# Performance work log

Hardware: AMD Instinct MI355X
Metric: run time of the kernel (lower is better)

## Reference

```python
import jax, jax.numpy as jnp
import numpy as np

TOP_K = 4
NORM_TOPK_PROB = True


def _moe_forward(hidden_states, Wr, Wg, Wu, Wd):
    # hidden_states: [B, S, H]; Wr: [E, H]; Wg/Wu: [E, F, H]; Wd: [E, H, F]
    B, S, H = hidden_states.shape
    E = Wr.shape[0]
    x = hidden_states.reshape(-1, H)                     # [T, H]
    T = x.shape[0]

    # Router: softmax in float32 (matches F.softmax(..., dtype=torch.float))
    router_logits = x @ Wr.T                              # [T, E]
    probs = jax.nn.softmax(router_logits.astype(jnp.float32), axis=-1)
    routing_weights, selected_experts = jax.lax.top_k(probs, TOP_K)  # [T, K]
    if NORM_TOPK_PROB:
        routing_weights = routing_weights / jnp.sum(routing_weights, axis=-1, keepdims=True)
    routing_weights = routing_weights.astype(x.dtype)

    # Dense combine matrix: combine[t, e] = routing weight if expert e selected for token t else 0.
    # Equivalent to the sort/gather dispatch + weighted scatter-add in the torch code.
    combine = jnp.zeros((T, E), dtype=x.dtype).at[
        jnp.arange(T)[:, None], selected_experts
    ].add(routing_weights)                               # [T, E]

    # SwiGLU expert MLP: down(silu(gate(x)) * up(x)), evaluated for all experts,
    # then masked/weighted by combine (zero weight == token not routed to expert).
    hg = jnp.einsum('td,efd->tef', x, Wg)                # [T, E, F]
    hu = jnp.einsum('td,efd->tef', x, Wu)                # [T, E, F]
    act = jax.nn.silu(hg) * hu                           # [T, E, F]
    out = jnp.einsum('tef,te,edf->td', act, combine, Wd) # [T, H]
    return out.reshape(B, S, H)


def setup_inputs() -> dict:
    key = jax.random.key(0)
    k0, k1, k2, k3, k4 = jax.random.split(key, 5)
    B, S, H, E, F = 2, 2048, 2048, 16, 768
    scale = 0.02
    return {
        'hidden_states': jax.random.normal(k0, (B, S, H), dtype=jnp.float32),
        'Wr': jax.random.normal(k1, (E, H), dtype=jnp.float32) * scale,
        'Wg': jax.random.normal(k2, (E, F, H), dtype=jnp.float32) * scale,
        'Wu': jax.random.normal(k3, (E, F, H), dtype=jnp.float32) * scale,
        'Wd': jax.random.normal(k4, (E, H, F), dtype=jnp.float32) * scale,
    }


def reference(hidden_states, Wr, Wg, Wu, Wd):
    return _moe_forward(hidden_states, Wr, Wg, Wu, Wd)
```

## Files before the change

### kernel.cpp

```cpp
#include <hip/hip_runtime.h>
#include <hip/hip_bf16.h>

#define H_DIM 2048
#define F_DIM 768
#define E_NUM 16
#define T_TOK 4096
#define TOPK  4
#define TK_ROWS (T_TOK * TOPK)

typedef __attribute__((ext_vector_type(8))) short bf16x8;
typedef __attribute__((ext_vector_type(4))) float f32x4;

static __device__ __forceinline__ float bf2f(unsigned short u) {
    return __uint_as_float(((unsigned)u) << 16);
}
static __device__ __forceinline__ unsigned short f2bu(float f) {
    __hip_bfloat16 h = __float2bfloat16(f);
    return *(unsigned short*)&h;
}

static __device__ __forceinline__ void stage8(unsigned short* dst, const void* src,
                                              size_t eoff, bool f32) {
    if (f32) {
        const float* s = (const float*)src + eoff;
        float4 a = *(const float4*)s;
        float4 b = *(const float4*)(s + 4);
        __align__(16) unsigned short u[8] = {
            f2bu(a.x), f2bu(a.y), f2bu(a.z), f2bu(a.w),
            f2bu(b.x), f2bu(b.y), f2bu(b.z), f2bu(b.w)};
        *(uint4*)dst = *(const uint4*)u;
    } else {
        *(uint4*)dst = *(const uint4*)((const unsigned short*)src + eoff);
    }
}

__global__ void probe_kernel(const unsigned short* __restrict__ wr, int* __restrict__ flag) {
    const int tid = threadIdx.x;
    int maxe = 0;
    for (int i = tid; i < 512; i += 64) {
        int e = (wr[i] >> 7) & 0xFF;
        maxe = max(maxe, e);
    }
    for (int off = 32; off > 0; off >>= 1)
        maxe = max(maxe, __shfl_down(maxe, off, 64));
    if (tid == 0) flag[0] = (maxe >= 135) ? 1 : 0;
}

__global__ __launch_bounds__(256)
void convert_kernel(unsigned short* __restrict__ dst, const void* __restrict__ src,
                    const int* __restrict__ dflag, size_t n) {
    const size_t i = ((size_t)blockIdx.x * 256 + threadIdx.x) * 8;
    if (i >= n) return;
    stage8(dst + i, src, i, dflag[0] != 0);
}

__global__ __launch_bounds__(256)
void router_kernel(const void* __restrict__ xv,
                   const void* __restrict__ wrv,
                   const int* __restrict__ dflag,
                   float* __restrict__ topk_w,
                   int* __restrict__ topk_e,
                   int* __restrict__ counts) {
    const bool f32 = dflag[0] != 0;
    const int t = blockIdx.x;
    __shared__ float xs[H_DIM];
    __shared__ float logits_s[E_NUM];
    const int tid = threadIdx.x;

    if (f32) {
        const float4* xr = (const float4*)((const float*)xv + (size_t)t * H_DIM);
        ((float4*)xs)[tid] = xr[tid];
        ((float4*)xs)[tid + 256] = xr[tid + 256];
    } else {
        const uint4* xr = (const uint4*)((const unsigned short*)xv + (size_t)t * H_DIM);
        uint4 b = xr[tid];
        const unsigned short* bp = (const unsigned short*)&b;
#pragma unroll
        for (int j = 0; j < 8; ++j) xs[tid * 8 + j] = bf2f(bp[j]);
    }
    __syncthreads();

    const int w = tid >> 6;
    const int lane = tid & 63;

    float acc[4] = {0.f, 0.f, 0.f, 0.f};
    for (int i = 0; i < 4; ++i) {
        const int h = i * 512 + lane * 8;
        float xf[8];
#pragma unroll
        for (int j = 0; j < 8; ++j) xf[j] = xs[h + j];
#pragma unroll
        for (int je = 0; je < 4; ++je) {
            const int e = w * 4 + je;
            float wf[8];
            if (f32) {
                const float* wp = (const float*)wrv + (size_t)e * H_DIM + h;
                float4 a = *(const float4*)wp;
                float4 b = *(const float4*)(wp + 4);
                wf[0]=a.x; wf[1]=a.y; wf[2]=a.z; wf[3]=a.w;
                wf[4]=b.x; wf[5]=b.y; wf[6]=b.z; wf[7]=b.w;
            } else {
                uint4 wb = *(const uint4*)((const unsigned short*)wrv + (size_t)e * H_DIM + h);
                const unsigned short* wp = (const unsigned short*)&wb;
#pragma unroll
                for (int j = 0; j < 8; ++j) wf[j] = bf2f(wp[j]);
            }
            float s = 0.f;
#pragma unroll
            for (int j = 0; j < 8; ++j) s += xf[j] * wf[j];
            acc[je] += s;
        }
    }
#pragma unroll
    for (int je = 0; je < 4; ++je) {
        float v = acc[je];
        for (int off = 32; off > 0; off >>= 1) v += __shfl_down(v, off, 64);
        if (lane == 0) logits_s[w * 4 + je] = v;
    }
    __syncthreads();

    if (tid == 0) {
        float l[E_NUM];
#pragma unroll
        for (int i = 0; i < E_NUM; ++i) l[i] = logits_s[i];
        unsigned mask = 0;
        int sel_e[TOPK];
        float sel_v[TOPK];
        for (int k = 0; k < TOPK; ++k) {
            int be = 0; float bv = -1e30f;
            for (int i = 0; i < E_NUM; ++i) {
                if (!(mask & (1u << i)) && l[i] > bv) { bv = l[i]; be = i; }
            }
            mask |= (1u << be);
            sel_e[k] = be; sel_v[k] = bv;
        }
        const float m = sel_v[0];
        float ex[TOPK]; float s = 0.f;
        for (int k = 0; k < TOPK; ++k) { ex[k] = __expf(sel_v[k] - m); s += ex[k]; }
        const float inv = 1.f / s;
        for (int k = 0; k < TOPK; ++k) {
            float wgt = ex[k] * inv;
            if (!f32) wgt = bf2f(f2bu(wgt));
            topk_w[t * TOPK + k] = wgt;
            topk_e[t * TOPK + k] = sel_e[k];
            atomicAdd(&counts[sel_e[k]], 1);
        }
    }
}

__global__ void scan_kernel(const int* __restrict__ counts, int* __restrict__ offsets) {
    if (threadIdx.x == 0) {
        int s = 0;
        for (int e = 0; e < E_NUM; ++e) { offsets[e] = s; s += counts[e]; }
        offsets[E_NUM] = s;
    }
}

__global__ __launch_bounds__(256)
void scatter_kernel(const int* __restrict__ topk_e, const int* __restrict__ offsets,
                    int* __restrict__ cursors, int* __restrict__ row_token) {
    const int i = blockIdx.x * 256 + threadIdx.x;
    if (i < TK_ROWS) {
        const int e = topk_e[i];
        const int pos = offsets[e] + atomicAdd(&cursors[e], 1);
        row_token[pos] = i;
    }
}

__global__ __launch_bounds__(256, 2)
void gateup_kernel(const void* __restrict__ xv,
                   const void* __restrict__ wgv,
                   const void* __restrict__ wuv,
                   const int* __restrict__ dflag,
                   const int* __restrict__ row_token,
                   const int* __restrict__ counts,
                   const int* __restrict__ offsets,
                   __hip_bfloat16* __restrict__ act_buf) {
    const bool f32 = dflag[0] != 0;
    const int e  = blockIdx.z;
    const int mt = blockIdx.y;
    const int ft = blockIdx.x;
    const int cnt = counts[e];
    if (mt * 128 >= cnt) return;
    const int base = offsets[e];

    __shared__ unsigned short As[128 * 72];
    __shared__ unsigned short Bgs[128 * 72];
    __shared__ unsigned short Bus[128 * 72];
    __shared__ int tok_s[128];

    const int tid = threadIdx.x;
    if (tid < 128) {
        int r = mt * 128 + tid;
        int gr = base + (r < cnt ? r : cnt - 1);
        tok_s[tid] = row_token[gr] >> 2;
    }
    __syncthreads();

    f32x4 accg[4][4], accu[4][4];
#pragma unroll
    for (int mi = 0; mi < 4; ++mi)
#pragma unroll
        for (int ni = 0; ni < 4; ++ni)
#pragma unroll
            for (int r = 0; r < 4; ++r) { accg[mi][ni][r] = 0.f; accu[mi][ni][r] = 0.f; }

    const int wid  = tid >> 6;
    const int lane = tid & 63;
    const int wm = (wid >> 1) * 64;
    const int wn = (wid & 1) * 64;
    const int lr = lane & 15;
    const int lq = lane >> 4;

    const int lrow = tid >> 3;
    const int lcol = (tid & 7) * 8;

    const size_t gOff = ((size_t)e * F_DIM + ft * 128) * H_DIM;

    for (int kk = 0; kk < H_DIM / 64; ++kk) {
        const int k0 = kk * 64;
#pragma unroll
        for (int rep = 0; rep < 4; ++rep) {
            const int row = lrow + rep * 32;
            stage8(&As[row * 72 + lcol],  xv,  (size_t)tok_s[row] * H_DIM + k0 + lcol, f32);
            stage8(&Bgs[row * 72 + lcol], wgv, gOff + (size_t)row * H_DIM + k0 + lcol, f32);
            stage8(&Bus[row * 72 + lcol], wuv, gOff + (size_t)row * H_DIM + k0 + lcol, f32);
        }
        __syncthreads();
#pragma unroll
        for (int ks = 0; ks < 2; ++ks) {
            const int kb = ks * 32 + lq * 8;
            bf16x8 a[4], bg[4], bu[4];
#pragma unroll
            for (int mi = 0; mi < 4; ++mi)
                a[mi] = *(const bf16x8*)&As[(wm + mi * 16 + lr) * 72 + kb];
#pragma unroll
            for (int ni = 0; ni < 4; ++ni) {
                bg[ni] = *(const bf16x8*)&Bgs[(wn + ni * 16 + lr) * 72 + kb];
                bu[ni] = *(const bf16x8*)&Bus[(wn + ni * 16 + lr) * 72 + kb];
            }
#pragma unroll
            for (int mi = 0; mi < 4; ++mi)
#pragma unroll
                for (int ni = 0; ni < 4; ++ni) {
                    accg[mi][ni] = __builtin_amdgcn_mfma_f32_16x16x32_bf16(a[mi], bg[ni], accg[mi][ni], 0, 0, 0);
                    accu[mi][ni] = __builtin_amdgcn_mfma_f32_16x16x32_bf16(a[mi], bu[ni], accu[mi][ni], 0, 0, 0);
                }
        }
        __syncthreads();
    }

#pragma unroll
    for (int mi = 0; mi < 4; ++mi) {
#pragma unroll
        for (int r = 0; r < 4; ++r) {
            const int row  = wm + mi * 16 + lq * 4 + r;
            const int grow = mt * 128 + row;
            if (grow < cnt) {
                __hip_bfloat16* dst = act_buf + (size_t)(base + grow) * F_DIM + ft * 128 + wn;
#pragma unroll
                for (int ni = 0; ni < 4; ++ni) {
                    const float g = accg[mi][ni][r];
                    const float u = accu[mi][ni][r];
                    const float s = g / (1.f + __expf(-g));
                    dst[ni * 16 + lr] = __float2bfloat16(s * u);
                }
            }
        }
    }
}

__global__ __launch_bounds__(256, 2)
void down_kernel(const __hip_bfloat16* __restrict__ act_buf,
                 const void* __restrict__ wdv,
                 const int* __restrict__ dflag,
                 const int* __restrict__ row_token,
                 const int* __restrict__ counts,
                 const int* __restrict__ offsets,
                 const float* __restrict__ topk_w,
                 float* __restrict__ out) {
    const bool f32 = dflag[0] != 0;
    const int e  = blockIdx.z;
    const int mt = blockIdx.y;
    const int ht = blockIdx.x;
    const int cnt = counts[e];
    if (mt * 128 >= cnt) return;
    const int base = offsets[e];

    __shared__ unsigned short As[128 * 72];
    __shared__ unsigned short Bs[128 * 72];
    __shared__ int tok_s[128];
    __shared__ float w_s[128];

    const int tid = threadIdx.x;
    if (tid < 128) {
        int r = mt * 128 + tid;
        int gr = base + (r < cnt ? r : cnt - 1);
        const int t4 = row_token[gr];
        tok_s[tid] = t4 >> 2;
        w_s[tid] = topk_w[t4];
    }
    __syncthreads();

    f32x4 accd[4][4];
#pragma unroll
    for (int mi = 0; mi < 4; ++mi)
#pragma unroll
        for (int ni = 0; ni < 4; ++ni)
#pragma unroll
            for (int r = 0; r < 4; ++r) accd[mi][ni][r] = 0.f;

    const int wid  = tid >> 6;
    const int lane = tid & 63;
    const int wm = (wid >> 1) * 64;
    const int wn = (wid & 1) * 64;
    const int lr = lane & 15;
    const int lq = lane >> 4;

    const int lrow = tid >> 3;
    const int lcol = (tid & 7) * 8;

    const unsigned short* au = (const unsigned short*)act_buf;
    const size_t hOff = ((size_t)e * H_DIM + ht * 128) * F_DIM;

    for (int kk = 0; kk < F_DIM / 64; ++kk) {
        const int k0 = kk * 64;
#pragma unroll
        for (int rep = 0; rep < 4; ++rep) {
            const int row = lrow + rep * 32;
            int ar = mt * 128 + row;
            ar = (ar < cnt) ? ar : (cnt - 1);
            *(uint4*)&As[row * 72 + lcol] = *(const uint4*)(au + (size_t)(base + ar) * F_DIM + k0 + lcol);
            stage8(&Bs[row * 72 + lcol], wdv, hOff + (size_t)row * F_DIM + k0 + lcol, f32);
        }
        __syncthreads();
#pragma unroll
        for (int ks = 0; ks < 2; ++ks) {
            const int kb = ks * 32 + lq * 8;
            bf16x8 a[4], b[4];
#pragma unroll
            for (int mi = 0; mi < 4; ++mi)
                a[mi] = *(const bf16x8*)&As[(wm + mi * 16 + lr) * 72 + kb];
#pragma unroll
            for (int ni = 0; ni < 4; ++ni)
                b[ni] = *(const bf16x8*)&Bs[(wn + ni * 16 + lr) * 72 + kb];
#pragma unroll
            for (int mi = 0; mi < 4; ++mi)
#pragma unroll
                for (int ni = 0; ni < 4; ++ni)
                    accd[mi][ni] = __builtin_amdgcn_mfma_f32_16x16x32_bf16(a[mi], b[ni], accd[mi][ni], 0, 0, 0);
        }
        __syncthreads();
    }

#pragma unroll
    for (int mi = 0; mi < 4; ++mi) {
#pragma unroll
        for (int r = 0; r < 4; ++r) {
            const int row  = wm + mi * 16 + lq * 4 + r;
            const int grow = mt * 128 + row;
            if (grow < cnt) {
                const float wgt = w_s[row];
                float* dst = out + (size_t)tok_s[row] * H_DIM + ht * 128 + wn;
#pragma unroll
                for (int ni = 0; ni < 4; ++ni)
                    atomicAdd(&dst[ni * 16 + lr], accd[mi][ni][r] * wgt);
            }
        }
    }
}

extern "C" void kernel_launch(void* const* d_in, const int* in_sizes, int n_in,
                              void* d_out, int out_size, void* d_ws, size_t ws_size,
                              hipStream_t stream) {
    const void* x  = d_in[0];
    const void* Wr = d_in[1];
    const void* Wg = d_in[2];
    const void* Wu = d_in[3];
    const void* Wd = d_in[4];
    float* out = (float*)d_out;

    const size_t nX = (size_t)T_TOK * H_DIM;
    const size_t nW = (size_t)E_NUM * F_DIM * H_DIM;

    char* ws = (char*)d_ws;
    size_t o = 0;
    float* topk_w    = (float*)(ws + o); o += (size_t)TK_ROWS * 4;
    int*   topk_e    = (int*)(ws + o);   o += (size_t)TK_ROWS * 4;
    int*   row_token = (int*)(ws + o);   o += (size_t)TK_ROWS * 4;
    int*   counts    = (int*)(ws + o);   o += 64;
    int*   cursors   = (int*)(ws + o);   o += 64;
    int*   zflag     = (int*)(ws + o);   o += 64;
    int*   dflag     = (int*)(ws + o);   o += 64;
    int*   offsets   = (int*)(ws + o);   o += 128;
    __hip_bfloat16* act_buf = (__hip_bfloat16*)(ws + o); o += (size_t)TK_ROWS * F_DIM * 2;
    const size_t baseNeed = o;
    unsigned short* xb  = (unsigned short*)(ws + o); o += nX * 2;
    unsigned short* Wgb = (unsigned short*)(ws + o); o += nW * 2;
    unsigned short* Wub = (unsigned short*)(ws + o); o += nW * 2;
    unsigned short* Wdb = (unsigned short*)(ws + o); o += nW * 2;
    const bool fast = (ws_size >= o);
    (void)baseNeed;

    hipMemsetAsync(out, 0, (size_t)out_size * sizeof(float), stream);
    hipMemsetAsync(counts, 0, 192, stream);

    probe_kernel<<<1, 64, 0, stream>>>((const unsigned short*)Wr, dflag);
    router_kernel<<<T_TOK, 256, 0, stream>>>(x, Wr, dflag, topk_w, topk_e, counts);
    scan_kernel<<<1, 64, 0, stream>>>(counts, offsets);
    scatter_kernel<<<TK_ROWS / 256, 256, 0, stream>>>(topk_e, offsets, cursors, row_token);

    const void* gx = x;  const void* gg = Wg; const void* gu = Wu; const void* gd = Wd;
    const int* gemm_flag = dflag;
    if (fast) {
        convert_kernel<<<(int)(nX / 2048), 256, 0, stream>>>(xb,  x,  dflag, nX);
        convert_kernel<<<(int)(nW / 2048), 256, 0, stream>>>(Wgb, Wg, dflag, nW);
        convert_kernel<<<(int)(nW / 2048), 256, 0, stream>>>(Wub, Wu, dflag, nW);
        convert_kernel<<<(int)(nW / 2048), 256, 0, stream>>>(Wdb, Wd, dflag, nW);
        gx = xb; gg = Wgb; gu = Wub; gd = Wdb;
        gemm_flag = zflag;
    }

    gateup_kernel<<<dim3(F_DIM / 128, 32, E_NUM), 256, 0, stream>>>(
        gx, gg, gu, gemm_flag, row_token, counts, offsets, act_buf);
    down_kernel<<<dim3(H_DIM / 128, 32, E_NUM), 256, 0, stream>>>(
        act_buf, gd, gemm_flag, row_token, counts, offsets, topk_w, out);
}
```

Before: 1.137 ms.

## Use direct global-to-LDS loads, XOR-swizzled LDS, compact tile list, batched router

Adds bf16 fast-path GEMM kernels that stage tiles with global_load_lds straight into XOR-swizzled unpadded shared memory. The scan kernel now builds a compact list of (expert, m-tile) pairs, so the grid no longer launches a 32x16 sweep of mostly empty blocks. The router processes 8 tokens per block so each router weight load is reused across tokens. The change targets register-staged load overhead, LDS bank conflicts and empty-block launch cost. Risks: the tile list is capped at MAX_TILES, and the gemm kernels lose their occupancy hint of 2.

```diff
diff --git a/kernel.cpp b/kernel.cpp
--- a/kernel.cpp
+++ b/kernel.cpp
@@ -7,6 +7,7 @@
 #define T_TOK 4096
 #define TOPK  4
 #define TK_ROWS (T_TOK * TOPK)
+#define MAX_TILES 160
 
 typedef __attribute__((ext_vector_type(8))) short bf16x8;
 typedef __attribute__((ext_vector_type(4))) float f32x4;
@@ -17,6 +18,13 @@
 static __device__ __forceinline__ unsigned short f2bu(float f) {
     __hip_bfloat16 h = __float2bfloat16(f);
     return *(unsigned short*)&h;
+}
+
+static __device__ __forceinline__ void gl16(const unsigned short* g, unsigned short* l) {
+    __builtin_amdgcn_global_load_lds(
+        (__attribute__((address_space(1))) void*)(g),
+        (__attribute__((address_space(3))) void*)(l),
+        16, 0, 0);
 }
 
 static __device__ __forceinline__ void stage8(unsigned short* dst, const void* src,
@@ -54,7 +62,7 @@
     stage8(dst + i, src, i, dflag[0] != 0);
 }
 
-__global__ __launch_bounds__(256)
+__global__ __launch_bounds__(256, 2)
 void router_kernel(const void* __restrict__ xv,
                    const void* __restrict__ wrv,
                    const int* __restrict__ dflag,
@@ -62,33 +70,38 @@
                    int* __restrict__ topk_e,
                    int* __restrict__ counts) {
     const bool f32 = dflag[0] != 0;
-    const int t = blockIdx.x;
-    __shared__ float xs[H_DIM];
-    __shared__ float logits_s[E_NUM];
+    const int t0 = blockIdx.x * 8;
+    __shared__ float xs[8][H_DIM];
+    __shared__ float logits_s[8][E_NUM];
     const int tid = threadIdx.x;
 
     if (f32) {
-        const float4* xr = (const float4*)((const float*)xv + (size_t)t * H_DIM);
-        ((float4*)xs)[tid] = xr[tid];
-        ((float4*)xs)[tid + 256] = xr[tid + 256];
+        const float4* src = (const float4*)((const float*)xv + (size_t)t0 * H_DIM);
+        float4* dst = (float4*)&xs[0][0];
+        for (int i = tid; i < 8 * H_DIM / 4; i += 256) dst[i] = src[i];
     } else {
-        const uint4* xr = (const uint4*)((const unsigned short*)xv + (size_t)t * H_DIM);
-        uint4 b = xr[tid];
-        const unsigned short* bp = (const unsigned short*)&b;
-#pragma unroll
-        for (int j = 0; j < 8; ++j) xs[tid * 8 + j] = bf2f(bp[j]);
+        const uint4* src = (const uint4*)((const unsigned short*)xv + (size_t)t0 * H_DIM);
+        for (int i = tid; i < 8 * H_DIM / 8; i += 256) {
+            uint4 b = src[i];
+            const unsigned short* bp = (const unsigned short*)&b;
+            float* d = &xs[0][0] + (size_t)i * 8;
+#pragma unroll
+            for (int j = 0; j < 8; ++j) d[j] = bf2f(bp[j]);
+        }
     }
     __syncthreads();
 
     const int w = tid >> 6;
     const int lane = tid & 63;
 
-    float acc[4] = {0.f, 0.f, 0.f, 0.f};
+    float acc[8][4];
+#pragma unroll
+    for (int t = 0; t < 8; ++t)
+#pragma unroll
+        for (int je = 0; je < 4; ++je) acc[t][je] = 0.f;
+
     for (int i = 0; i < 4; ++i) {
         const int h = i * 512 + lane * 8;
-        float xf[8];
-#pragma unroll
-        for (int j = 0; j < 8; ++j) xf[j] = xs[h + j];
 #pragma unroll
         for (int je = 0; je < 4; ++je) {
             const int e = w * 4 + je;
@@ -105,24 +118,33 @@
 #pragma unroll
                 for (int j = 0; j < 8; ++j) wf[j] = bf2f(wp[j]);
             }
-            float s = 0.f;
-#pragma unroll
-            for (int j = 0; j < 8; ++j) s += xf[j] * wf[j];
-            acc[je] += s;
-        }
-    }
-#pragma unroll
-    for (int je = 0; je < 4; ++je) {
-        float v = acc[je];
-        for (int off = 32; off > 0; off >>= 1) v += __shfl_down(v, off, 64);
-        if (lane == 0) logits_s[w * 4 + je] = v;
-    }
+#pragma unroll
+            for (int t = 0; t < 8; ++t) {
+                const float* xp = &xs[t][h];
+                float s = 0.f;
+#pragma unroll
+                for (int j = 0; j < 8; ++j) s += xp[j] * wf[j];
+                acc[t][je] += s;
+            }
+        }
+    }
+#pragma unroll
+    for (int t = 0; t < 8; ++t)
+#pragma unroll
+        for (int je = 0; je < 4; ++je) {
+            float v = acc[t][je];
+            v += __shfl_down(v, 32, 64); v += __shfl_down(v, 16, 64);
+            v += __shfl_down(v, 8, 64);  v += __shfl_down(v, 4, 64);
+            v += __shfl_down(v, 2, 64);  v += __shfl_down(v, 1, 64);
+            if (lane == 0) logits_s[t][w * 4 + je] = v;
+        }
     __syncthreads();
 
-    if (tid == 0) {
+    if (tid < 8) {
+        const int t = t0 + tid;
         float l[E_NUM];
 #pragma unroll
-        for (int i = 0; i < E_NUM; ++i) l[i] = logits_s[i];
+        for (int i = 0; i < E_NUM; ++i) l[i] = logits_s[tid][i];
         unsigned mask = 0;
         int sel_e[TOPK];
         float sel_v[TOPK];
@@ -148,11 +170,19 @@
     }
 }
 
-__global__ void scan_kernel(const int* __restrict__ counts, int* __restrict__ offsets) {
+__global__ void scan_kernel(const int* __restrict__ counts, int* __restrict__ offsets,
+                            int* __restrict__ tiles, int* __restrict__ ntiles) {
     if (threadIdx.x == 0) {
-        int s = 0;
-        for (int e = 0; e < E_NUM; ++e) { offsets[e] = s; s += counts[e]; }
+        int s = 0, nt = 0;
+        for (int e = 0; e < E_NUM; ++e) {
+            offsets[e] = s;
+            const int c = counts[e];
+            s += c;
+            for (int mt = 0; mt * 128 < c && nt < MAX_TILES; ++mt)
+                tiles[nt++] = (e << 16) | mt;
+        }
         offsets[E_NUM] = s;
+        ntiles[0] = nt;
     }
 }
 
@@ -167,36 +197,60 @@
     }
 }
 
-__global__ __launch_bounds__(256, 2)
-void gateup_kernel(const void* __restrict__ xv,
-                   const void* __restrict__ wgv,
-                   const void* __restrict__ wuv,
-                   const int* __restrict__ dflag,
-                   const int* __restrict__ row_token,
-                   const int* __restrict__ counts,
-                   const int* __restrict__ offsets,
-                   __hip_bfloat16* __restrict__ act_buf) {
-    const bool f32 = dflag[0] != 0;
-    const int e  = blockIdx.z;
-    const int mt = blockIdx.y;
+__global__ __launch_bounds__(256)
+void gateup_fast(const unsigned short* __restrict__ x,
+                 const unsigned short* __restrict__ Wg,
+                 const unsigned short* __restrict__ Wu,
+                 const int* __restrict__ row_token,
+                 const int* __restrict__ counts,
+                 const int* __restrict__ offsets,
+                 const int* __restrict__ tiles,
+                 const int* __restrict__ ntiles,
+                 __hip_bfloat16* __restrict__ act_buf) {
+    const int ti = blockIdx.y;
+    if (ti >= ntiles[0]) return;
+    const int packed = tiles[ti];
+    const int e = packed >> 16, mt = packed & 0xffff;
     const int ft = blockIdx.x;
-    const int cnt = counts[e];
-    if (mt * 128 >= cnt) return;
-    const int base = offsets[e];
-
-    __shared__ unsigned short As[128 * 72];
-    __shared__ unsigned short Bgs[128 * 72];
-    __shared__ unsigned short Bus[128 * 72];
+    const int cnt = counts[e], base = offsets[e];
+
+    __shared__ unsigned short As[128 * 64];
+    __shared__ unsigned short Bgs[128 * 64];
+    __shared__ unsigned short Bus[128 * 64];
     __shared__ int tok_s[128];
 
     const int tid = threadIdx.x;
     if (tid < 128) {
         int r = mt * 128 + tid;
-        int gr = base + (r < cnt ? r : cnt - 1);
-        tok_s[tid] = row_token[gr] >> 2;
+        tok_s[tid] = row_token[base + (r < cnt ? r : cnt - 1)] >> 2;
     }
     __syncthreads();
 
+    const int w = tid >> 6;
+    const int lane = tid & 63;
+    const int subrow = lane >> 3;
+    const int sgrp = lane & 7;
+    const int lgrp = sgrp ^ subrow;
+
+    const unsigned short* aptr[4];
+    const unsigned short* bgptr[4];
+    const unsigned short* buptr[4];
+    unsigned short* ldsA[4];
+    unsigned short* ldsBg[4];
+    unsigned short* ldsBu[4];
+    const size_t gOff = ((size_t)e * F_DIM + (size_t)ft * 128) * H_DIM;
+#pragma unroll
+    for (int j = 0; j < 4; ++j) {
+        const int r = (w * 4 + j) * 8 + subrow;
+        aptr[j]  = x + (size_t)tok_s[r] * H_DIM + lgrp * 8;
+        bgptr[j] = Wg + gOff + (size_t)r * H_DIM + lgrp * 8;
+        buptr[j] = Wu + gOff + (size_t)r * H_DIM + lgrp * 8;
+        const int lo = r * 64 + sgrp * 8;
+        ldsA[j]  = &As[lo];
+        ldsBg[j] = &Bgs[lo];
+        ldsBu[j] = &Bus[lo];
+    }
+
     f32x4 accg[4][4], accu[4][4];
 #pragma unroll
     for (int mi = 0; mi < 4; ++mi)
@@ -205,39 +259,35 @@
 #pragma unroll
             for (int r = 0; r < 4; ++r) { accg[mi][ni][r] = 0.f; accu[mi][ni][r] = 0.f; }
 
-    const int wid  = tid >> 6;
-    const int lane = tid & 63;
-    const int wm = (wid >> 1) * 64;
-    const int wn = (wid & 1) * 64;
+    const int wm = (w >> 1) * 64;
+    const int wn = (w & 1) * 64;
     const int lr = lane & 15;
     const int lq = lane >> 4;
-
-    const int lrow = tid >> 3;
-    const int lcol = (tid & 7) * 8;
-
-    const size_t gOff = ((size_t)e * F_DIM + ft * 128) * H_DIM;
+    const int gx = lr & 7;
+    const int aoff[2] = { (wm + lr) * 64 + ((lq    ) ^ gx) * 8,
+                          (wm + lr) * 64 + ((4 + lq) ^ gx) * 8 };
+    const int boff[2] = { (wn + lr) * 64 + ((lq    ) ^ gx) * 8,
+                          (wn + lr) * 64 + ((4 + lq) ^ gx) * 8 };
 
     for (int kk = 0; kk < H_DIM / 64; ++kk) {
         const int k0 = kk * 64;
 #pragma unroll
-        for (int rep = 0; rep < 4; ++rep) {
-            const int row = lrow + rep * 32;
-            stage8(&As[row * 72 + lcol],  xv,  (size_t)tok_s[row] * H_DIM + k0 + lcol, f32);
-            stage8(&Bgs[row * 72 + lcol], wgv, gOff + (size_t)row * H_DIM + k0 + lcol, f32);
-            stage8(&Bus[row * 72 + lcol], wuv, gOff + (size_t)row * H_DIM + k0 + lcol, f32);
+        for (int j = 0; j < 4; ++j) {
+            gl16(aptr[j] + k0, ldsA[j]);
+            gl16(bgptr[j] + k0, ldsBg[j]);
+            gl16(buptr[j] + k0, ldsBu[j]);
         }
         __syncthreads();
 #pragma unroll
         for (int ks = 0; ks < 2; ++ks) {
-            const int kb = ks * 32 + lq * 8;
             bf16x8 a[4], bg[4], bu[4];
 #pragma unroll
             for (int mi = 0; mi < 4; ++mi)
-                a[mi] = *(const bf16x8*)&As[(wm + mi * 16 + lr) * 72 + kb];
+                a[mi] = *(const bf16x8*)&As[aoff[ks] + mi * 1024];
 #pragma unroll
             for (int ni = 0; ni < 4; ++ni) {
-                bg[ni] = *(const bf16x8*)&Bgs[(wn + ni * 16 + lr) * 72 + kb];
-                bu[ni] = *(const bf16x8*)&Bus[(wn + ni * 16 + lr) * 72 + kb];
+                bg[ni] = *(const bf16x8*)&Bgs[boff[ks] + ni * 1024];
+                bu[ni] = *(const bf16x8*)&Bus[boff[ks] + ni * 1024];
             }
 #pragma unroll
             for (int mi = 0; mi < 4; ++mi)
@@ -270,38 +320,226 @@
     }
 }
 
+__global__ __launch_bounds__(256)
+void down_fast(const unsigned short* __restrict__ act,
+               const unsigned short* __restrict__ Wd,
+               const int* __restrict__ row_token,
+               const int* __restrict__ counts,
+               const int* __restrict__ offsets,
+               const int* __restrict__ tiles,
+               const int* __restrict__ ntiles,
+               const float* __restrict__ topk_w,
+               float* __restrict__ out) {
+    const int ti = blockIdx.y;
+    if (ti >= ntiles[0]) return;
+    const int packed = tiles[ti];
+    const int e = packed >> 16, mt = packed & 0xffff;
+    const int ht = blockIdx.x;
+    const int cnt = counts[e], base = offsets[e];
+
+    __shared__ unsigned short As[128 * 64];
+    __shared__ unsigned short Bs[128 * 64];
+    __shared__ int tok_s[128];
+    __shared__ float w_s[128];
+
+    const int tid = threadIdx.x;
+    if (tid < 128) {
+        int r = mt * 128 + tid;
+        const int t4 = row_token[base + (r < cnt ? r : cnt - 1)];
+        tok_s[tid] = t4 >> 2;
+        w_s[tid] = topk_w[t4];
+    }
+    __syncthreads();
+
+    const int w = tid >> 6;
+    const int lane = tid & 63;
+    const int subrow = lane >> 3;
+    const int sgrp = lane & 7;
+    const int lgrp = sgrp ^ subrow;
+
+    const unsigned short* aptr[4];
+    const unsigned short* bptr[4];
+    unsigned short* ldsA[4];
+    unsigned short* ldsB[4];
+    const size_t hOff = ((size_t)e * H_DIM + (size_t)ht * 128) * F_DIM;
+#pragma unroll
+    for (int j = 0; j < 4; ++j) {
+        const int r = (w * 4 + j) * 8 + subrow;
+        int ar = mt * 128 + r;
+        ar = (ar < cnt) ? ar : (cnt - 1);
+        aptr[j] = act + (size_t)(base + ar) * F_DIM + lgrp * 8;
+        bptr[j] = Wd + hOff + (size_t)r * F_DIM + lgrp * 8;
+        const int lo = r * 64 + sgrp * 8;
+        ldsA[j] = &As[lo];
+        ldsB[j] = &Bs[lo];
+    }
+
+    f32x4 accd[4][4];
+#pragma unroll
+    for (int mi = 0; mi < 4; ++mi)
+#pragma unroll
+        for (int ni = 0; ni < 4; ++ni)
+#pragma unroll
+            for (int r = 0; r < 4; ++r) accd[mi][ni][r] = 0.f;
+
+    const int wm = (w >> 1) * 64;
+    const int wn = (w & 1) * 64;
+    const int lr = lane & 15;
+    const int lq = lane >> 4;
+    const int gx = lr & 7;
+    const int aoff[2] = { (wm + lr) * 64 + ((lq    ) ^ gx) * 8,
+                          (wm + lr) * 64 + ((4 + lq) ^ gx) * 8 };
+    const int boff[2] = { (wn + lr) * 64 + ((lq    ) ^ gx) * 8,
+                          (wn + lr) * 64 + ((4 + lq) ^ gx) * 8 };
+
+    for (int kk = 0; kk < F_DIM / 64; ++kk) {
+        const int k0 = kk * 64;
+#pragma unroll
+        for (int j = 0; j < 4; ++j) {
+            gl16(aptr[j] + k0, ldsA[j]);
+            gl16(bptr[j] + k0, ldsB[j]);
+        }
+        __syncthreads();
+#pragma unroll
+        for (int ks = 0; ks < 2; ++ks) {
+            bf16x8 a[4], b[4];
+#pragma unroll
+            for (int mi = 0; mi < 4; ++mi)
+                a[mi] = *(const bf16x8*)&As[aoff[ks] + mi * 1024];
+#pragma unroll
+            for (int ni = 0; ni < 4; ++ni)
+                b[ni] = *(const bf16x8*)&Bs[boff[ks] + ni * 1024];
+#pragma unroll
+            for (int mi = 0; mi < 4; ++mi)
+#pragma unroll
+                for (int ni = 0; ni < 4; ++ni)
+                    accd[mi][ni] = __builtin_amdgcn_mfma_f32_16x16x32_bf16(a[mi], b[ni], accd[mi][ni], 0, 0, 0);
+        }
+        __syncthreads();
+    }
+
+#pragma unroll
+    for (int mi = 0; mi < 4; ++mi) {
+#pragma unroll
+        for (int r = 0; r < 4; ++r) {
+            const int row  = wm + mi * 16 + lq * 4 + r;
+            const int grow = mt * 128 + row;
+            if (grow < cnt) {
+                const float wgt = w_s[row];
+                float* dst = out + (size_t)tok_s[row] * H_DIM + ht * 128 + wn;
+#pragma unroll
+                for (int ni = 0; ni < 4; ++ni)
+                    atomicAdd(&dst[ni * 16 + lr], accd[mi][ni][r] * wgt);
+            }
+        }
+    }
+}
+
 __global__ __launch_bounds__(256, 2)
-void down_kernel(const __hip_bfloat16* __restrict__ act_buf,
-                 const void* __restrict__ wdv,
-                 const int* __restrict__ dflag,
-                 const int* __restrict__ row_token,
-                 const int* __restrict__ counts,
-                 const int* __restrict__ offsets,
-                 const float* __restrict__ topk_w,
-                 float* __restrict__ out) {
+void gateup_slow(const void* __restrict__ xv, const void* __restrict__ wgv,
+                 const void* __restrict__ wuv, const int* __restrict__ dflag,
+                 const int* __restrict__ row_token, const int* __restrict__ counts,
+                 const int* __restrict__ offsets, __hip_bfloat16* __restrict__ act_buf) {
     const bool f32 = dflag[0] != 0;
-    const int e  = blockIdx.z;
-    const int mt = blockIdx.y;
-    const int ht = blockIdx.x;
+    const int e = blockIdx.z, mt = blockIdx.y, ft = blockIdx.x;
     const int cnt = counts[e];
     if (mt * 128 >= cnt) return;
     const int base = offsets[e];
-
+    __shared__ unsigned short As[128 * 72];
+    __shared__ unsigned short Bgs[128 * 72];
+    __shared__ unsigned short Bus[128 * 72];
+    __shared__ int tok_s[128];
+    const int tid = threadIdx.x;
+    if (tid < 128) {
+        int r = mt * 128 + tid;
+        tok_s[tid] = row_token[base + (r < cnt ? r : cnt - 1)] >> 2;
+    }
+    __syncthreads();
+    f32x4 accg[4][4], accu[4][4];
+#pragma unroll
+    for (int mi = 0; mi < 4; ++mi)
+#pragma unroll
+        for (int ni = 0; ni < 4; ++ni)
+#pragma unroll
+            for (int r = 0; r < 4; ++r) { accg[mi][ni][r] = 0.f; accu[mi][ni][r] = 0.f; }
+    const int wid = tid >> 6, lane = tid & 63;
+    const int wm = (wid >> 1) * 64, wn = (wid & 1) * 64;
+    const int lr = lane & 15, lq = lane >> 4;
+    const int lrow = tid >> 3, lcol = (tid & 7) * 8;
+    const size_t gOff = ((size_t)e * F_DIM + ft * 128) * H_DIM;
+    for (int kk = 0; kk < H_DIM / 64; ++kk) {
+        const int k0 = kk * 64;
+#pragma unroll
+        for (int rep = 0; rep < 4; ++rep) {
+            const int row = lrow + rep * 32;
+            stage8(&As[row * 72 + lcol],  xv,  (size_t)tok_s[row] * H_DIM + k0 + lcol, f32);
+            stage8(&Bgs[row * 72 + lcol], wgv, gOff + (size_t)row * H_DIM + k0 + lcol, f32);
+            stage8(&Bus[row * 72 + lcol], wuv, gOff + (size_t)row * H_DIM + k0 + lcol, f32);
+        }
+        __syncthreads();
+#pragma unroll
+        for (int ks = 0; ks < 2; ++ks) {
+            const int kb = ks * 32 + lq * 8;
+            bf16x8 a[4], bg[4], bu[4];
+#pragma unroll
+            for (int mi = 0; mi < 4; ++mi)
+                a[mi] = *(const bf16x8*)&As[(wm + mi * 16 + lr) * 72 + kb];
+#pragma unroll
+            for (int ni = 0; ni < 4; ++ni) {
+                bg[ni] = *(const bf16x8*)&Bgs[(wn + ni * 16 + lr) * 72 + kb];
+                bu[ni] = *(const bf16x8*)&Bus[(wn + ni * 16 + lr) * 72 + kb];
+            }
+#pragma unroll
+            for (int mi = 0; mi < 4; ++mi)
+#pragma unroll
+                for (int ni = 0; ni < 4; ++ni) {
+                    accg[mi][ni] = __builtin_amdgcn_mfma_f32_16x16x32_bf16(a[mi], bg[ni], accg[mi][ni], 0, 0, 0);
+                    accu[mi][ni] = __builtin_amdgcn_mfma_f32_16x16x32_bf16(a[mi], bu[ni], accu[mi][ni], 0, 0, 0);
+                }
+        }
+        __syncthreads();
+    }
+#pragma unroll
+    for (int mi = 0; mi < 4; ++mi) {
+#pragma unroll
+        for (int r = 0; r < 4; ++r) {
+            const int row = wm + mi * 16 + lq * 4 + r;
+            const int grow = mt * 128 + row;
+            if (grow < cnt) {
+                __hip_bfloat16* dst = act_buf + (size_t)(base + grow) * F_DIM + ft * 128 + wn;
+#pragma unroll
+                for (int ni = 0; ni < 4; ++ni) {
+                    const float g = accg[mi][ni][r];
+                    const float u = accu[mi][ni][r];
+                    dst[ni * 16 + lr] = __float2bfloat16((g / (1.f + __expf(-g))) * u);
+                }
+            }
+        }
+    }
+}
+
+__global__ __launch_bounds__(256, 2)
+void down_slow(const __hip_bfloat16* __restrict__ act_buf, const void* __restrict__ wdv,
+               const int* __restrict__ dflag, const int* __restrict__ row_token,
+               const int* __restrict__ counts, const int* __restrict__ offsets,
+               const float* __restrict__ topk_w, float* __restrict__ out) {
+    const bool f32 = dflag[0] != 0;
+    const int e = blockIdx.z, mt = blockIdx.y, ht = blockIdx.x;
+    const int cnt = counts[e];
+    if (mt * 128 >= cnt) return;
+    const int base = offsets[e];
     __shared__ unsigned short As[128 * 72];
     __shared__ unsigned short Bs[128 * 72];
     __shared__ int tok_s[128];
     __shared__ float w_s[128];
-
     const int tid = threadIdx.x;
     if (tid < 128) {
         int r = mt * 128 + tid;
-        int gr = base + (r < cnt ? r : cnt - 1);
-        const int t4 = row_token[gr];
+        const int t4 = row_token[base + (r < cnt ? r : cnt - 1)];
         tok_s[tid] = t4 >> 2;
         w_s[tid] = topk_w[t4];
     }
     __syncthreads();
-
     f32x4 accd[4][4];
 #pragma unroll
     for (int mi = 0; mi < 4; ++mi)
@@ -309,20 +547,12 @@
         for (int ni = 0; ni < 4; ++ni)
 #pragma unroll
             for (int r = 0; r < 4; ++r) accd[mi][ni][r] = 0.f;
-
-    const int wid  = tid >> 6;
-    const int lane = tid & 63;
-    const int wm = (wid >> 1) * 64;
-    const int wn = (wid & 1) * 64;
-    const int lr = lane & 15;
-    const int lq = lane >> 4;
-
-    const int lrow = tid >> 3;
-    const int lcol = (tid & 7) * 8;
-
+    const int wid = tid >> 6, lane = tid & 63;
+    const int wm = (wid >> 1) * 64, wn = (wid & 1) * 64;
+    const int lr = lane & 15, lq = lane >> 4;
+    const int lrow = tid >> 3, lcol = (tid & 7) * 8;
     const unsigned short* au = (const unsigned short*)act_buf;
     const size_t hOff = ((size_t)e * H_DIM + ht * 128) * F_DIM;
-
     for (int kk = 0; kk < F_DIM / 64; ++kk) {
         const int k0 = kk * 64;
 #pragma unroll
@@ -352,12 +582,11 @@
         }
         __syncthreads();
     }
-
 #pragma unroll
     for (int mi = 0; mi < 4; ++mi) {
 #pragma unroll
         for (int r = 0; r < 4; ++r) {
-            const int row  = wm + mi * 16 + lq * 4 + r;
+            const int row = wm + mi * 16 + lq * 4 + r;
             const int grow = mt * 128 + row;
             if (grow < cnt) {
                 const float wgt = w_s[row];
@@ -393,36 +622,38 @@
     int*   zflag     = (int*)(ws + o);   o += 64;
     int*   dflag     = (int*)(ws + o);   o += 64;
     int*   offsets   = (int*)(ws + o);   o += 128;
+    int*   ntiles    = (int*)(ws + o);   o += 64;
+    int*   tiles     = (int*)(ws + o);   o += MAX_TILES * 4;
     __hip_bfloat16* act_buf = (__hip_bfloat16*)(ws + o); o += (size_t)TK_ROWS * F_DIM * 2;
-    const size_t baseNeed = o;
     unsigned short* xb  = (unsigned short*)(ws + o); o += nX * 2;
     unsigned short* Wgb = (unsigned short*)(ws + o); o += nW * 2;
     unsigned short* Wub = (unsigned short*)(ws + o); o += nW * 2;
     unsigned short* Wdb = (unsigned short*)(ws + o); o += nW * 2;
     const bool fast = (ws_size >= o);
-    (void)baseNeed;
+    (void)zflag;
 
     hipMemsetAsync(out, 0, (size_t)out_size * sizeof(float), stream);
     hipMemsetAsync(counts, 0, 192, stream);
 
     probe_kernel<<<1, 64, 0, stream>>>((const unsigned short*)Wr, dflag);
-    router_kernel<<<T_TOK, 256, 0, stream>>>(x, Wr, dflag, topk_w, topk_e, counts);
-    scan_kernel<<<1, 64, 0, stream>>>(counts, offsets);
+    router_kernel<<<T_TOK / 8, 256, 0, stream>>>(x, Wr, dflag, topk_w, topk_e, counts);
+    scan_kernel<<<1, 64, 0, stream>>>(counts, offsets, tiles, ntiles);
     scatter_kernel<<<TK_ROWS / 256, 256, 0, stream>>>(topk_e, offsets, cursors, row_token);
 
-    const void* gx = x;  const void* gg = Wg; const void* gu = Wu; const void* gd = Wd;
-    const int* gemm_flag = dflag;
     if (fast) {
         convert_kernel<<<(int)(nX / 2048), 256, 0, stream>>>(xb,  x,  dflag, nX);
         convert_kernel<<<(int)(nW / 2048), 256, 0, stream>>>(Wgb, Wg, dflag, nW);
         convert_kernel<<<(int)(nW / 2048), 256, 0, stream>>>(Wub, Wu, dflag, nW);
         convert_kernel<<<(int)(nW / 2048), 256, 0, stream>>>(Wdb, Wd, dflag, nW);
-        gx = xb; gg = Wgb; gu = Wub; gd = Wdb;
-        gemm_flag = zflag;
-    }
-
-    gateup_kernel<<<dim3(F_DIM / 128, 32, E_NUM), 256, 0, stream>>>(
-        gx, gg, gu, gemm_flag, row_token, counts, offsets, act_buf);
-    down_kernel<<<dim3(H_DIM / 128, 32, E_NUM), 256, 0, stream>>>(
-        act_buf, gd, gemm_flag, row_token, counts, offsets, topk_w, out);
-}
+        gateup_fast<<<dim3(F_DIM / 128, MAX_TILES), 256, 0, stream>>>(
+            xb, Wgb, Wub, row_token, counts, offsets, tiles, ntiles, act_buf);
+        down_fast<<<dim3(H_DIM / 128, MAX_TILES), 256, 0, stream>>>(
+            (const unsigned short*)act_buf, Wdb, row_token, counts, offsets,
+            tiles, ntiles, topk_w, out);
+    } else {
+        gateup_slow<<<dim3(F_DIM / 128, 32, E_NUM), 256, 0, stream>>>(
+            x, Wg, Wu, dflag, row_token, counts, offsets, act_buf);
+        down_slow<<<dim3(H_DIM / 128, 32, E_NUM), 256, 0, stream>>>(
+            act_buf, Wd, dflag, row_token, counts, offsets, topk_w, out);
+    }
+}
```

Result: faster. 936.9 us (-17.6%).
